# Optimization experiments

Measured on AMD Instinct MI355X. Metric: run time of the kernel, lower is better.

## Reference

```python
import jax, jax.numpy as jnp
import numpy as np
from jax import lax

B, D, C, K = 8192, 512, 1000, 8
EPS = 1e-8
TEMP = 0.2
NEG = -10000.0


def setup_inputs() -> dict:
    key = jax.random.key(0)
    ks = jax.random.split(key, 6)
    z = jax.random.normal(ks[0], (B, D), dtype=jnp.float32)
    n_exp = jax.random.randint(ks[1], (B,), 0, K, dtype=jnp.int32)
    s1 = 1.0 / np.sqrt(D)
    W1 = jax.random.normal(ks[2], (K, D, D), dtype=jnp.float32) * s1
    b1 = jax.random.normal(ks[3], (K, D), dtype=jnp.float32) * 0.01
    W2 = jax.random.normal(ks[4], (K, D, C), dtype=jnp.float32) * s1
    b2 = jax.random.normal(ks[5], (K, C), dtype=jnp.float32) * 0.01
    return {"z": z, "n_exp": n_exp, "W1": W1, "b1": b1, "W2": W2, "b2": b2}


def _gates_one(p, c, n):
    # p: [K,C] softmax probs for one sample; c: [K] confidences; n: scalar int
    pn = p / (jnp.linalg.norm(p, axis=-1, keepdims=True) + EPS)
    S = pn @ pn.T  # [K,K] pairwise cosine similarity
    sel0 = jnp.zeros((K,), dtype=bool).at[jnp.argmax(c)].set(True)

    def body(t, sel):
        # max cosine sim of each candidate to already-selected set
        max_sim = jnp.max(jnp.where(sel[None, :], S, -jnp.inf), axis=1)
        dist = jnp.where(sel, -jnp.inf, 1.0 - max_sim)
        new = sel.at[jnp.argmax(dist)].set(True)
        return jnp.where(t < n, new, sel)

    sel = lax.fori_loop(1, K, body, sel0)
    gate_logits = jnp.where(sel, c, NEG) / TEMP
    return jax.nn.softmax(gate_logits)


def reference(z, n_exp, W1, b1, W2, b2):
    # K expert MLPs, batched: [B,d] -> [B,K,C]
    h = jax.nn.relu(jnp.einsum('bd,kde->bke', z, W1) + b1[None])
    logits_all = jnp.einsum('bke,kec->bkc', h, W2) + b2[None]
    probs = jax.nn.softmax(logits_all, axis=-1)
    conf = jnp.max(probs, axis=-1)  # [B,K]
    gates = jax.vmap(_gates_one)(probs, conf, n_exp)  # [B,K]
    logits = jnp.einsum('bkc,bk->bc', logits_all, gates)
    return logits, gates
```

## Files before the change

kernel.cpp:

```cpp
#include <hip/hip_runtime.h>
#include <math.h>

#define B_SZ 8192
#define D_DIM 512
#define C_DIM 1000
#define C_PAD 1024
#define K_EXP 8
#define TEMP_INV 5.0f
#define EPS_N 1e-8f

typedef __attribute__((ext_vector_type(8))) short frag_ab;
typedef __attribute__((ext_vector_type(4))) float frag_cd;

__device__ __forceinline__ short f2bf(float f) {
    unsigned u = __builtin_bit_cast(unsigned, f);
    unsigned r = (u + 0x7fffu + ((u >> 16) & 1u)) >> 16;
    return (short)r;
}
__device__ __forceinline__ float bf2f(short s) {
    unsigned u = ((unsigned)(unsigned short)s) << 16;
    return __builtin_bit_cast(float, u);
}
__device__ __forceinline__ void split2(float v, short& s0, short& s1) {
    s0 = f2bf(v);
    s1 = f2bf(v - bf2f(s0));
}

__device__ __forceinline__ void gl_lds16(const short* g, short* l) {
    __builtin_amdgcn_global_load_lds(
        (const __attribute__((address_space(1))) unsigned int*)(const void*)g,
        (__attribute__((address_space(3))) unsigned int*)(void*)l,
        16, 0, 0);
}

__global__ __launch_bounds__(256) void prep_z(const float* __restrict__ z,
                                              short* __restrict__ p0, short* __restrict__ p1) {
    int idx = blockIdx.x * 256 + threadIdx.x;
    float v = z[idx];
    short a, b; split2(v, a, b);
    p0[idx] = a; p1[idx] = b;
}

__global__ __launch_bounds__(256) void prep_w1t(const float* __restrict__ W1,
                                                short* __restrict__ p0, short* __restrict__ p1) {
    __shared__ float t[32][33];
    const int k = blockIdx.z;
    const int d0 = blockIdx.x * 32;
    const int e0 = blockIdx.y * 32;
    const int tx = threadIdx.x & 31, ty = threadIdx.x >> 5;
    const float* src = W1 + ((size_t)k << 18);
#pragma unroll
    for (int r = 0; r < 4; r++) {
        int d = d0 + ty + 8 * r;
        t[ty + 8 * r][tx] = src[(size_t)d * 512 + e0 + tx];
    }
    __syncthreads();
#pragma unroll
    for (int r = 0; r < 4; r++) {
        int e = e0 + ty + 8 * r;
        int d = d0 + tx;
        float v = t[tx][ty + 8 * r];
        short a, b; split2(v, a, b);
        size_t o = ((size_t)k << 18) + (size_t)e * 512 + d;
        p0[o] = a; p1[o] = b;
    }
}

__global__ __launch_bounds__(256) void prep_w2t(const float* __restrict__ W2,
                                                short* __restrict__ p0, short* __restrict__ p1) {
    __shared__ float t[32][33];
    const int k = blockIdx.z;
    const int e0 = blockIdx.x * 32;
    const int c0 = blockIdx.y * 32;
    const int tx = threadIdx.x & 31, ty = threadIdx.x >> 5;
    const float* src = W2 + (size_t)k * (D_DIM * C_DIM);
#pragma unroll
    for (int r = 0; r < 4; r++) {
        int e = e0 + ty + 8 * r;
        int c = c0 + tx;
        t[ty + 8 * r][tx] = (c < C_DIM) ? src[(size_t)e * C_DIM + c] : 0.f;
    }
    __syncthreads();
#pragma unroll
    for (int r = 0; r < 4; r++) {
        int c = c0 + ty + 8 * r;
        int e = e0 + tx;
        float v = t[tx][ty + 8 * r];
        short a, b; split2(v, a, b);
        size_t o = (size_t)k * (C_PAD * D_DIM) + (size_t)c * 512 + e;
        p0[o] = a; p1[o] = b;
    }
}

__global__ __launch_bounds__(256, 2) void gemm_split(
    const short* __restrict__ A0, const short* __restrict__ A1, long long aBatch,
    const short* __restrict__ B0, const short* __restrict__ B1, long long bBatch,
    const float* __restrict__ bias, int biasBatch,
    float* __restrict__ Cf, long long cBatch, int ldc, int Nout,
    short* __restrict__ H0, short* __restrict__ H1, long long hBatch,
    int mt, int nt, int mode)
{
    const int lin = blockIdx.x;
    const int k = lin & 7;
    const int rem = lin >> 3;
    const int gm = (mt >= 2) ? 2 : 1;
    const int win = rem / (gm * nt);
    const int local = rem % (gm * nt);
    const int m0 = (win * gm + local / nt) * 256;
    const int n0 = (local % nt) * 128;

    const int tid = threadIdx.x;
    const int lane = tid & 63;
    const int wv = tid >> 6;
    const int wm = (wv & 1) * 128;
    const int wn = (wv >> 1) * 64;

    __shared__ short lds[24576];

    const short* gA0 = A0 + (size_t)k * aBatch + (size_t)m0 * 512;
    const short* gA1 = A1 + (size_t)k * aBatch + (size_t)m0 * 512;
    const short* gB0 = B0 + (size_t)k * bBatch + (size_t)n0 * 512;
    const short* gB1 = B1 + (size_t)k * bBatch + (size_t)n0 * 512;
    short* ldsA = lds;
    short* ldsB = lds + 16384;

    frag_cd acc[8][4];
#pragma unroll
    for (int i = 0; i < 8; i++)
#pragma unroll
        for (int j = 0; j < 4; j++)
            acc[i][j] = (frag_cd){0.f, 0.f, 0.f, 0.f};

    const int srow = tid >> 2;
    const int sc   = tid & 3;

    for (int k0 = 0; k0 < 512; k0 += 32) {
        const short* ga[2] = {gA0, gA1};
        const short* gb[2] = {gB0, gB1};
#pragma unroll
        for (int p = 0; p < 2; p++) {
#pragma unroll
            for (int hh = 0; hh < 4; hh++) {
                int row = hh * 64 + srow;
                int gq = sc ^ ((row >> 1) & 3);
                gl_lds16(ga[p] + (size_t)row * 512 + k0 + gq * 8,
                         ldsA + p * 8192 + row * 32 + sc * 8);
            }
#pragma unroll
            for (int hh = 0; hh < 2; hh++) {
                int row = hh * 64 + srow;
                int gq = sc ^ ((row >> 1) & 3);
                gl_lds16(gb[p] + (size_t)row * 512 + k0 + gq * 8,
                         ldsB + p * 4096 + row * 32 + sc * 8);
            }
        }
        __syncthreads();

        const int q = lane >> 4;
        const int rb = lane & 15;

        frag_ab bfr[2][4];
#pragma unroll
        for (int p = 0; p < 2; p++)
#pragma unroll
            for (int j = 0; j < 4; j++) {
                int R = wn + j * 16 + rb;
                int slot = q ^ ((R >> 1) & 3);
                bfr[p][j] = *(const frag_ab*)(ldsB + p * 4096 + R * 32 + slot * 8);
            }

#pragma unroll
        for (int i = 0; i < 8; i++) {
            int R = wm + i * 16 + rb;
            int slot = q ^ ((R >> 1) & 3);
            frag_ab a0 = *(const frag_ab*)(ldsA + R * 32 + slot * 8);
            frag_ab a1 = *(const frag_ab*)(ldsA + 8192 + R * 32 + slot * 8);
#pragma unroll
            for (int j = 0; j < 4; j++) {
                frag_cd c = acc[i][j];
                c = __builtin_amdgcn_mfma_f32_16x16x32_bf16(a0, bfr[0][j], c, 0, 0, 0);
                c = __builtin_amdgcn_mfma_f32_16x16x32_bf16(a0, bfr[1][j], c, 0, 0, 0);
                c = __builtin_amdgcn_mfma_f32_16x16x32_bf16(a1, bfr[0][j], c, 0, 0, 0);
                acc[i][j] = c;
            }
        }
        __syncthreads();
    }

    const int r0 = (lane >> 4) * 4;
    const int cc = lane & 15;
    if (mode == 0) {
        float* C = Cf + (size_t)k * cBatch;
        const float* bb = bias + (size_t)k * biasBatch;
#pragma unroll
        for (int i = 0; i < 8; i++) {
            int rowb = m0 + wm + i * 16 + r0;
#pragma unroll
            for (int j = 0; j < 4; j++) {
                int col = n0 + wn + j * 16 + cc;
                if (col < Nout) {
                    float b = bb[col];
#pragma unroll
                    for (int r = 0; r < 4; r++)
                        C[(size_t)(rowb + r) * ldc + col] = acc[i][j][r] + b;
                }
            }
        }
    } else {
        short* h0 = H0 + (size_t)k * hBatch;
        short* h1 = H1 + (size_t)k * hBatch;
        const float* bb = bias + (size_t)k * biasBatch;
#pragma unroll
        for (int i = 0; i < 8; i++) {
            int rowb = m0 + wm + i * 16 + r0;
#pragma unroll
            for (int j = 0; j < 4; j++) {
                int col = n0 + wn + j * 16 + cc;
                float b = bb[col];
#pragma unroll
                for (int r = 0; r < 4; r++) {
                    float v = fmaxf(acc[i][j][r] + b, 0.f);
                    short s0, s1; split2(v, s0, s1);
                    size_t o = (size_t)(rowb + r) * 512 + col;
                    h0[o] = s0; h1[o] = s1;
                }
            }
        }
    }
}

__global__ __launch_bounds__(256) void gate_combine(
    const float* __restrict__ L,
    const int* __restrict__ n_exp,
    float* __restrict__ out_logits,
    float* __restrict__ out_gates,
    int Bc)
{
    const int wv = threadIdx.x >> 6;
    const int lane = threadIdx.x & 63;
    const int b = blockIdx.x * 4 + wv;
    const size_t kcs = (size_t)Bc * C_DIM;
    const float* Lb = L + (size_t)b * C_DIM;

    __shared__ float Sm[4][64];
    __shared__ float Zm[4][8];

    float mx[K_EXP], Zs[K_EXP], dd[36];
#pragma unroll
    for (int k = 0; k < K_EXP; k++) { mx[k] = -INFINITY; Zs[k] = 0.f; }
#pragma unroll
    for (int p = 0; p < 36; p++) dd[p] = 0.f;

    for (int c = lane; c < C_DIM; c += 64) {
        float e[K_EXP];
#pragma unroll
        for (int k = 0; k < K_EXP; k++) {
            float l = Lb[(size_t)k * kcs + c];
            mx[k] = fmaxf(mx[k], l);
            e[k] = __expf(l);
            Zs[k] += e[k];
        }
        int idx = 0;
#pragma unroll
        for (int i = 0; i < K_EXP; i++)
#pragma unroll
            for (int j = i; j < K_EXP; j++) {
                dd[idx] = fmaf(e[i], e[j], dd[idx]);
                idx++;
            }
    }

#pragma unroll
    for (int off = 32; off > 0; off >>= 1) {
#pragma unroll
        for (int k = 0; k < K_EXP; k++) {
            mx[k] = fmaxf(mx[k], __shfl_xor(mx[k], off, 64));
            Zs[k] += __shfl_xor(Zs[k], off, 64);
        }
#pragma unroll
        for (int p = 0; p < 36; p++)
            dd[p] += __shfl_xor(dd[p], off, 64);
    }

    if (lane == 0) {
        int idx = 0;
#pragma unroll
        for (int i = 0; i < K_EXP; i++)
#pragma unroll
            for (int j = i; j < K_EXP; j++) {
                Sm[wv][i * 8 + j] = dd[idx];
                Sm[wv][j * 8 + i] = dd[idx];
                idx++;
            }
#pragma unroll
        for (int k = 0; k < K_EXP; k++) Zm[wv][k] = Zs[k];
    }

    const int ti = lane >> 3, tj = lane & 7;
    const float Zi = Zm[wv][ti], Zj = Zm[wv][tj];
    const float dij = Sm[wv][ti * 8 + tj];
    const float dii = Sm[wv][ti * 8 + ti];
    const float djj = Sm[wv][tj * 8 + tj];
    const float ni = sqrtf(dii) / Zi + EPS_N;
    const float nj = sqrtf(djj) / Zj + EPS_N;
    const float cosij = (dij / (Zi * Zj)) / (ni * nj);

    float conf[K_EXP];
#pragma unroll
    for (int k = 0; k < K_EXP; k++) conf[k] = __expf(mx[k]) / Zs[k];

    int i0 = 0; float bcf = conf[0];
#pragma unroll
    for (int k = 1; k < K_EXP; k++)
        if (conf[k] > bcf) { bcf = conf[k]; i0 = k; }
    unsigned sel = 1u << i0;
    const int n = n_exp[b];

    for (int t = 1; t < K_EXP; t++) {
        float v = ((sel >> tj) & 1u) ? cosij : -INFINITY;
        v = fmaxf(v, __shfl_xor(v, 1, 64));
        v = fmaxf(v, __shfl_xor(v, 2, 64));
        v = fmaxf(v, __shfl_xor(v, 4, 64));
        float dist = ((sel >> ti) & 1u) ? -INFINITY : 1.0f - v;
        float bv = dist; int bi = ti;
#pragma unroll
        for (int off = 8; off < 64; off <<= 1) {
            float ov = __shfl_xor(bv, off, 64);
            int oi = __shfl_xor(bi, off, 64);
            if (ov > bv || (ov == bv && oi < bi)) { bv = ov; bi = oi; }
        }
        if (t < n) sel |= 1u << bi;
    }

    float cmax = -INFINITY;
#pragma unroll
    for (int k = 0; k < K_EXP; k++)
        if ((sel >> k) & 1u) cmax = fmaxf(cmax, conf[k]);
    float g[K_EXP], gsum = 0.f;
#pragma unroll
    for (int k = 0; k < K_EXP; k++) {
        g[k] = ((sel >> k) & 1u) ? __expf((conf[k] - cmax) * TEMP_INV) : 0.f;
        gsum += g[k];
    }
    const float ginv = 1.0f / gsum;
#pragma unroll
    for (int k = 0; k < K_EXP; k++) g[k] *= ginv;

    if (lane == 0) {
        float4* og = (float4*)(out_gates + (size_t)b * K_EXP);
        og[0] = make_float4(g[0], g[1], g[2], g[3]);
        og[1] = make_float4(g[4], g[5], g[6], g[7]);
    }

    for (int c = lane; c < C_DIM; c += 64) {
        float o = 0.f;
#pragma unroll
        for (int k = 0; k < K_EXP; k++)
            o = fmaf(g[k], Lb[(size_t)k * kcs + c], o);
        out_logits[(size_t)b * C_DIM + c] = o;
    }
}

extern "C" void kernel_launch(void* const* d_in, const int* in_sizes, int n_in,
                              void* d_out, int out_size, void* d_ws, size_t ws_size,
                              hipStream_t stream) {
    const float* z     = (const float*)d_in[0];
    const int*   n_exp = (const int*)d_in[1];
    const float* W1    = (const float*)d_in[2];
    const float* b1    = (const float*)d_in[3];
    const float* W2    = (const float*)d_in[4];
    const float* b2    = (const float*)d_in[5];
    float* out_logits = (float*)d_out;
    float* out_gates  = (float*)d_out + (size_t)B_SZ * C_DIM;

    const size_t zP   = (size_t)B_SZ * D_DIM * 2;
    const size_t w1P  = (size_t)K_EXP * D_DIM * D_DIM * 2;
    const size_t w2P  = (size_t)K_EXP * C_PAD * D_DIM * 2;
    const size_t fixedBytes = 2 * (zP + w1P + w2P);

    int nch = 1;
    while (nch < 32 && fixedBytes + (size_t)(B_SZ / nch) * 48384 > ws_size) nch *= 2;
    const int Bc = B_SZ / nch;

    char* w = (char*)d_ws;
    short* zp[2];  zp[0]  = (short*)w; zp[1]  = (short*)(w + zP);  w += 2 * zP;
    short* w1t[2]; w1t[0] = (short*)w; w1t[1] = (short*)(w + w1P); w += 2 * w1P;
    short* w2t[2]; w2t[0] = (short*)w; w2t[1] = (short*)(w + w2P); w += 2 * w2P;
    const size_t hP = (size_t)K_EXP * Bc * D_DIM * 2;
    short* hp[2];  hp[0]  = (short*)w; hp[1]  = (short*)(w + hP);  w += 2 * hP;
    float* Lb = (float*)w;

    prep_z <<<dim3((B_SZ * D_DIM) / 256), 256, 0, stream>>>(z, zp[0], zp[1]);
    prep_w1t<<<dim3(16, 16, K_EXP), 256, 0, stream>>>(W1, w1t[0], w1t[1]);
    prep_w2t<<<dim3(16, 32, K_EXP), 256, 0, stream>>>(W2, w2t[0], w2t[1]);

    const int mt = Bc / 256;

    for (int ch = 0; ch < nch; ch++) {
        const int off = ch * Bc;
        const long long zoff = (long long)off * D_DIM;

        gemm_split<<<dim3(8 * mt * 4), 256, 0, stream>>>(
            zp[0] + zoff, zp[1] + zoff, 0LL,
            w1t[0], w1t[1], (long long)D_DIM * D_DIM,
            b1, D_DIM,
            nullptr, 0LL, 0, D_DIM,
            hp[0], hp[1], (long long)Bc * D_DIM,
            mt, 4, 1);

        gemm_split<<<dim3(8 * mt * 8), 256, 0, stream>>>(
            hp[0], hp[1], (long long)Bc * D_DIM,
            w2t[0], w2t[1], (long long)C_PAD * D_DIM,
            b2, C_DIM,
            Lb, (long long)Bc * C_DIM, C_DIM, C_DIM,
            nullptr, nullptr, 0LL,
            mt, 8, 0);

        gate_combine<<<dim3(Bc / 4), 256, 0, stream>>>(
            Lb, n_exp + off,
            out_logits + (size_t)off * C_DIM,
            out_gates + (size_t)off * K_EXP,
            Bc);
    }
}
```

Measured before the change: 496.9 us.

## Double-buffer LDS in split-bf16 GEMM with larger 256x256 tiles and 512 threads

Widens each GEMM block to a 256x256 output tile using 8 waves (512 threads) and halves the grid. Replaces the single-buffered K loop with a two-stage LDS ping-pong that issues the next k-slice's global-to-LDS loads before computing the current one, waiting with partial vmcnt. Also raises wave priority around the MFMA section. This aims to hide global load latency and raise reuse per LDS load, at the cost of 128KB of shared memory per block and fewer blocks resident per CU.

```diff
diff --git a/kernel.cpp b/kernel.cpp
--- a/kernel.cpp
+++ b/kernel.cpp
@@ -92,7 +92,7 @@
     }
 }
 
-__global__ __launch_bounds__(256, 2) void gemm_split(
+__global__ __launch_bounds__(512, 2) void gemm_split(
     const short* __restrict__ A0, const short* __restrict__ A1, long long aBatch,
     const short* __restrict__ B0, const short* __restrict__ B1, long long bBatch,
     const float* __restrict__ bias, int biasBatch,
@@ -107,7 +107,7 @@
     const int win = rem / (gm * nt);
     const int local = rem % (gm * nt);
     const int m0 = (win * gm + local / nt) * 256;
-    const int n0 = (local % nt) * 128;
+    const int n0 = (local % nt) * 256;
 
     const int tid = threadIdx.x;
     const int lane = tid & 63;
@@ -115,14 +115,14 @@
     const int wm = (wv & 1) * 128;
     const int wn = (wv >> 1) * 64;
 
-    __shared__ short lds[24576];
+    __shared__ short lds[65536];
 
     const short* gA0 = A0 + (size_t)k * aBatch + (size_t)m0 * 512;
     const short* gA1 = A1 + (size_t)k * aBatch + (size_t)m0 * 512;
     const short* gB0 = B0 + (size_t)k * bBatch + (size_t)n0 * 512;
     const short* gB1 = B1 + (size_t)k * bBatch + (size_t)n0 * 512;
-    short* ldsA = lds;
-    short* ldsB = lds + 16384;
+    const short* ga[2] = {gA0, gA1};
+    const short* gb[2] = {gB0, gB1};
 
     frag_cd acc[8][4];
 #pragma unroll
@@ -134,31 +134,27 @@
     const int srow = tid >> 2;
     const int sc   = tid & 3;
 
-    for (int k0 = 0; k0 < 512; k0 += 32) {
-        const short* ga[2] = {gA0, gA1};
-        const short* gb[2] = {gB0, gB1};
-#pragma unroll
-        for (int p = 0; p < 2; p++) {
-#pragma unroll
-            for (int hh = 0; hh < 4; hh++) {
-                int row = hh * 64 + srow;
-                int gq = sc ^ ((row >> 1) & 3);
-                gl_lds16(ga[p] + (size_t)row * 512 + k0 + gq * 8,
-                         ldsA + p * 8192 + row * 32 + sc * 8);
-            }
-#pragma unroll
-            for (int hh = 0; hh < 2; hh++) {
-                int row = hh * 64 + srow;
-                int gq = sc ^ ((row >> 1) & 3);
-                gl_lds16(gb[p] + (size_t)row * 512 + k0 + gq * 8,
-                         ldsB + p * 4096 + row * 32 + sc * 8);
-            }
-        }
-        __syncthreads();
-
-        const int q = lane >> 4;
-        const int rb = lane & 15;
-
+#define STAGE(KK0, BUFO) do {                                                   \
+    _Pragma("unroll")                                                           \
+    for (int p = 0; p < 2; p++) {                                               \
+        _Pragma("unroll")                                                       \
+        for (int hh = 0; hh < 2; hh++) {                                        \
+            int row = hh * 128 + srow;                                          \
+            int gq = sc ^ ((row >> 1) & 3);                                     \
+            gl_lds16(ga[p] + (size_t)row * 512 + (KK0) + gq * 8,                \
+                     lds + (BUFO) + p * 8192 + row * 32 + sc * 8);              \
+            gl_lds16(gb[p] + (size_t)row * 512 + (KK0) + gq * 8,                \
+                     lds + 32768 + (BUFO) + p * 8192 + row * 32 + sc * 8);      \
+        }                                                                       \
+    }                                                                           \
+} while (0)
+
+    const int q = lane >> 4;
+    const int rb = lane & 15;
+
+    auto compute = [&](int bufo) {
+        const short* bA = lds + bufo;
+        const short* bB = lds + 32768 + bufo;
         frag_ab bfr[2][4];
 #pragma unroll
         for (int p = 0; p < 2; p++)
@@ -166,15 +162,15 @@
             for (int j = 0; j < 4; j++) {
                 int R = wn + j * 16 + rb;
                 int slot = q ^ ((R >> 1) & 3);
-                bfr[p][j] = *(const frag_ab*)(ldsB + p * 4096 + R * 32 + slot * 8);
-            }
-
+                bfr[p][j] = *(const frag_ab*)(bB + p * 8192 + R * 32 + slot * 8);
+            }
+        __builtin_amdgcn_s_setprio(1);
 #pragma unroll
         for (int i = 0; i < 8; i++) {
             int R = wm + i * 16 + rb;
             int slot = q ^ ((R >> 1) & 3);
-            frag_ab a0 = *(const frag_ab*)(ldsA + R * 32 + slot * 8);
-            frag_ab a1 = *(const frag_ab*)(ldsA + 8192 + R * 32 + slot * 8);
+            frag_ab a0 = *(const frag_ab*)(bA + R * 32 + slot * 8);
+            frag_ab a1 = *(const frag_ab*)(bA + 8192 + R * 32 + slot * 8);
 #pragma unroll
             for (int j = 0; j < 4; j++) {
                 frag_cd c = acc[i][j];
@@ -184,8 +180,25 @@
                 acc[i][j] = c;
             }
         }
-        __syncthreads();
-    }
+        __builtin_amdgcn_s_setprio(0);
+    };
+
+    STAGE(0, 0);
+
+    for (int t = 0; t < 15; t++) {
+        STAGE((t + 1) * 32, ((t + 1) & 1) * 16384);
+        asm volatile("s_waitcnt vmcnt(8)" ::: "memory");
+        __builtin_amdgcn_s_barrier();
+        __builtin_amdgcn_sched_barrier(0);
+        compute((t & 1) * 16384);
+        __builtin_amdgcn_sched_barrier(0);
+        __builtin_amdgcn_s_barrier();
+    }
+    asm volatile("s_waitcnt vmcnt(0)" ::: "memory");
+    __builtin_amdgcn_s_barrier();
+    __builtin_amdgcn_sched_barrier(0);
+    compute(16384);
+#undef STAGE
 
     const int r0 = (lane >> 4) * 4;
     const int cc = lane & 15;
@@ -400,21 +413,21 @@
         const int off = ch * Bc;
         const long long zoff = (long long)off * D_DIM;
 
-        gemm_split<<<dim3(8 * mt * 4), 256, 0, stream>>>(
+        gemm_split<<<dim3(8 * mt * 2), 512, 0, stream>>>(
             zp[0] + zoff, zp[1] + zoff, 0LL,
             w1t[0], w1t[1], (long long)D_DIM * D_DIM,
             b1, D_DIM,
             nullptr, 0LL, 0, D_DIM,
             hp[0], hp[1], (long long)Bc * D_DIM,
-            mt, 4, 1);
-
-        gemm_split<<<dim3(8 * mt * 8), 256, 0, stream>>>(
+            mt, 2, 1);
+
+        gemm_split<<<dim3(8 * mt * 4), 512, 0, stream>>>(
             hp[0], hp[1], (long long)Bc * D_DIM,
             w2t[0], w2t[1], (long long)C_PAD * D_DIM,
             b2, C_DIM,
             Lb, (long long)Bc * C_DIM, C_DIM, C_DIM,
             nullptr, nullptr, 0LL,
-            mt, 8, 0);
+            mt, 4, 0);
 
         gate_combine<<<dim3(Bc / 4), 256, 0, stream>>>(
             Lb, n_exp + off,
```

After: 493.5 us. About the same (-0.7%).
